# Kernel tuning notes

Measured on AMD Instinct MI355X. Metric: run time of the kernel, lower is better.

## Reference

```python
import jax, jax.numpy as jnp
import numpy as np

EPS = 1e-12  # matches torch F.normalize eps


def _l2_normalize(x):
    # F.normalize(x, p=2, dim=1): divide by clamped norm
    norm = jnp.sqrt(jnp.sum(x * x, axis=1, keepdims=True))
    return x / jnp.maximum(norm, EPS)


def setup_inputs() -> dict:
    key = jax.random.key(0)
    k1, k2, k3 = jax.random.split(key, 3)
    N, D, P, C = 16384, 768, 2048, 1000
    h = jax.random.normal(k1, (N, D), dtype=jnp.float32)
    prototypes = jax.random.normal(k2, (P, D), dtype=jnp.float32) * 0.1
    prototype_class = jax.random.normal(k3, (P, C), dtype=jnp.float32)
    temperature = jnp.float32(1.0)
    return {"h": h, "prototypes": prototypes,
            "prototype_class": prototype_class, "temperature": temperature}


def reference(h, prototypes, prototype_class, temperature):
    h_norm = _l2_normalize(h)                      # [N, D]
    p_norm = _l2_normalize(prototypes)             # [P, D]
    # cdist (p=2): sqrt(||a||^2 + ||b||^2 - 2 a.b), clamped at 0
    h_sq = jnp.sum(h_norm * h_norm, axis=1, keepdims=True)   # [N, 1]
    p_sq = jnp.sum(p_norm * p_norm, axis=1)                  # [P]
    dots = jnp.einsum('nd,pd->np', h_norm, p_norm)           # [N, P]
    dist_sq = jnp.maximum(h_sq + p_sq[None, :] - 2.0 * dots, 0.0)
    distances = jnp.sqrt(dist_sq)                            # [N, P]
    tau = jax.nn.softplus(temperature)
    activations = jnp.exp(-tau * distances)                  # [N, P]
    class_logits = jnp.matmul(activations, prototype_class)  # [N, C]
    return class_logits
```

## Files before the change

### kernel.cpp

```cpp
#include <hip/hip_runtime.h>
#include <hip/hip_bf16.h>
#include <math.h>

typedef unsigned short ushort_t;
typedef unsigned char uchar_t;
typedef unsigned int uint_t;
typedef __attribute__((ext_vector_type(8))) short bf16x8;
typedef __attribute__((ext_vector_type(4))) float f32x4;
typedef __attribute__((ext_vector_type(2))) long longx2;

#define AS1 __attribute__((address_space(1)))
#define AS3 __attribute__((address_space(3)))

__device__ __forceinline__ void gld_lds16(const void* g, void* l) {
  __builtin_amdgcn_global_load_lds((const AS1 void*)g, (AS3 void*)l, 16, 0, 0);
}

__device__ __forceinline__ ushort_t f32_to_bf16_bits(float v) {
  __hip_bfloat16 b = __float2bfloat16(v);
  return *(ushort_t*)&b;
}

__device__ __forceinline__ uint_t pack_fp8x4(float4 v, float sc) {
  int r = __builtin_amdgcn_cvt_pk_fp8_f32(v.x * sc, v.y * sc, 0, false);
  r = __builtin_amdgcn_cvt_pk_fp8_f32(v.z * sc, v.w * sc, r, true);
  return (uint_t)r;
}


__global__ __launch_bounds__(256) void prep(const float4* __restrict__ h,
                                            uchar_t* __restrict__ h8, int rowsH,
                                            const float4* __restrict__ p,
                                            uchar_t* __restrict__ p8, int rowsP,
                                            const float* __restrict__ pc,
                                            ushort_t* __restrict__ pcT,
                                            int P, int C, int normBlocks) {
  __shared__ float tile[32][33];
  if ((int)blockIdx.x < normBlocks) {
    int r = (blockIdx.x * 256 + threadIdx.x) >> 6;
    const int lane = threadIdx.x & 63;
    const float4* xr;
    uchar_t* o8;
    if (r < rowsH) {
      xr = h + (size_t)r * 192;
      o8 = h8;
    } else {
      r -= rowsH;
      if (r >= rowsP) return;
      xr = p + (size_t)r * 192;
      o8 = p8;
    }
    float4 v0 = xr[lane];
    float4 v1 = xr[lane + 64];
    float4 v2 = xr[lane + 128];
    float ss = v0.x * v0.x + v0.y * v0.y + v0.z * v0.z + v0.w * v0.w
             + v1.x * v1.x + v1.y * v1.y + v1.z * v1.z + v1.w * v1.w
             + v2.x * v2.x + v2.y * v2.y + v2.z * v2.z + v2.w * v2.w;
#pragma unroll
    for (int off = 32; off > 0; off >>= 1) ss += __shfl_xor(ss, off, 64);
    const float sc = 4.0f / fmaxf(sqrtf(ss), 1e-12f);
    const int rb = r >> 4, rl = r & 15;
    const int key4 = (rl >> 1) & 3;
    const int u = (lane & 7) >> 1;
    const int ksub = (lane & 15) >> 3;
    const int cphys = ((u ^ key4) << 4) + (ksub << 3) + ((lane & 1) << 2);
    const int ktb = lane >> 4;
    uchar_t* rowbase = o8 + (size_t)rb * 12 * 1024 + rl * 64 + cphys;
    *(uint_t*)(rowbase + (size_t)(ktb) * 1024)     = pack_fp8x4(v0, sc);
    *(uint_t*)(rowbase + (size_t)(4 + ktb) * 1024) = pack_fp8x4(v1, sc);
    *(uint_t*)(rowbase + (size_t)(8 + ktb) * 1024) = pack_fp8x4(v2, sc);
  } else {
    const int b = blockIdx.x - normBlocks;
    const int nkb = P / 32;
    const int bk = b % nkb, bc = b / nkb;
    const int k0 = bk * 32, c0 = bc * 32;
    const int tx = threadIdx.x & 31, ty = threadIdx.x >> 5;
#pragma unroll
    for (int rr = 0; rr < 4; ++rr) {
      const int c = c0 + tx;
      tile[ty + rr * 8][tx] = (c < C) ? pc[(size_t)(k0 + ty + rr * 8) * C + c] : 0.f;
    }
    __syncthreads();
    const int c2 = tx >> 3, off = tx & 7;
#pragma unroll
    for (int rr = 0; rr < 4; ++rr) {
      const int row = c0 + ty + rr * 8;
      const int rb = row >> 4, rl = row & 15;
      const int key4 = (rl >> 1) & 3;
      size_t us = (((size_t)rb * nkb + bk) * 16 + rl) * 32 + ((c2 ^ key4) << 3) + off;
      pcT[us] = f32_to_bf16_bits(tile[tx][ty + rr * 8]);
    }
  }
}

#define BARRIER() do { asm volatile("" ::: "memory"); __builtin_amdgcn_s_barrier(); \
                       asm volatile("" ::: "memory"); } while (0)
#define LGKM0()   asm volatile("s_waitcnt lgkmcnt(0)" ::: "memory")
#define VM3()     asm volatile("s_waitcnt vmcnt(3)" ::: "memory")
#define VM0()     asm volatile("s_waitcnt vmcnt(0)" ::: "memory")
#define PRIO1()   __builtin_amdgcn_s_setprio(1)
#define PRIO0()   __builtin_amdgcn_s_setprio(0)
#define MM(a, b, c)  __builtin_amdgcn_mfma_f32_16x16x32_bf16(a, b, c, 0, 0, 0)
#define MM8(a, b, c) __builtin_amdgcn_mfma_f32_16x16x32_fp8_fp8(a, b, c, 0, 0, 0)

__launch_bounds__(512, 4)
__global__ void gemm1_fp8_t3(const uchar_t* __restrict__ A, const uchar_t* __restrict__ B,
                             ushort_t* __restrict__ act, const float* __restrict__ tptr,
                             int nKt, int actKT, int gx, int gxlog2) {
  __shared__ __align__(16) uchar_t sm1[73728];
  const int tid = threadIdx.x, lane = tid & 63, wave = tid >> 6;
  const int wm = wave >> 2, wn = wave & 3;
  const int lid = blockIdx.x, xcd = lid & 7, q = lid >> 3;
  const int tb = q & (gx - 1), sb = ((q >> gxlog2) << 3) | xcd;

  f32x4 acc[4][4];
#pragma unroll
  for (int i = 0; i < 4; ++i)
#pragma unroll
    for (int j = 0; j < 4; ++j) acc[i][j] = (f32x4){0.f, 0.f, 0.f, 0.f};

  const uchar_t* Apl = A + (((size_t)(sb * 8) * nKt) << 10) + lane * 16;
  const uchar_t* Bpl = B + (((size_t)(tb * 16) * nKt) << 10) + lane * 16;

  const int fr = lane & 15, g = lane >> 4;
  const int rdoff = fr * 64 + ((g ^ ((fr >> 1) & 3)) << 4);
  const uchar_t* smA = sm1 + (wm << 12) + rdoff;
  const uchar_t* smB = sm1 + 8192 + (wn << 12) + rdoff;

#define G1_STA(r_, T_, bo_) gld_lds16(Apl + ((size_t)((r_) * nKt + (T_)) << 10), \
                                      sm1 + (bo_) + ((r_) << 10))
#define G1_STB(c_, T_, bo_) gld_lds16(Bpl + ((size_t)((c_) * nKt + (T_)) << 10), \
                                      sm1 + (bo_) + 8192 + ((c_) << 10))
#define G1_DSA(bo_, i_) (*(const longx2*)(smA + (bo_) + ((i_) << 10)))
#define G1_DSB(bo_, j_) (*(const longx2*)(smB + (bo_) + ((j_) << 10)))

  G1_STA(wave, 0, 0); G1_STB(wave, 0, 0); G1_STB(wave + 8, 0, 0);
  G1_STA(wave, 1, 24576); G1_STB(wave, 1, 24576); G1_STB(wave + 8, 1, 24576);
  VM3(); BARRIER();

  int boC = 0, boN = 24576, boNN = 49152;
  for (int kt = 0; kt < nKt; ++kt) {
    longx2 a0 = G1_DSA(boC, 0), a1 = G1_DSA(boC, 1), a2 = G1_DSA(boC, 2), a3 = G1_DSA(boC, 3);
    longx2 b0 = G1_DSB(boC, 0), b1 = G1_DSB(boC, 1), b2 = G1_DSB(boC, 2), b3 = G1_DSB(boC, 3);
    if (kt + 2 < nKt) {
      G1_STA(wave, kt + 2, boNN); G1_STB(wave, kt + 2, boNN); G1_STB(wave + 8, kt + 2, boNN);
    }
    BARRIER(); LGKM0();
    PRIO1();
    acc[0][0] = MM8(a0[0], b0[0], acc[0][0]); acc[0][1] = MM8(a0[0], b1[0], acc[0][1]);
    acc[0][2] = MM8(a0[0], b2[0], acc[0][2]); acc[0][3] = MM8(a0[0], b3[0], acc[0][3]);
    acc[1][0] = MM8(a1[0], b0[0], acc[1][0]); acc[1][1] = MM8(a1[0], b1[0], acc[1][1]);
    acc[1][2] = MM8(a1[0], b2[0], acc[1][2]); acc[1][3] = MM8(a1[0], b3[0], acc[1][3]);
    acc[2][0] = MM8(a2[0], b0[0], acc[2][0]); acc[2][1] = MM8(a2[0], b1[0], acc[2][1]);
    acc[2][2] = MM8(a2[0], b2[0], acc[2][2]); acc[2][3] = MM8(a2[0], b3[0], acc[2][3]);
    acc[3][0] = MM8(a3[0], b0[0], acc[3][0]); acc[3][1] = MM8(a3[0], b1[0], acc[3][1]);
    acc[3][2] = MM8(a3[0], b2[0], acc[3][2]); acc[3][3] = MM8(a3[0], b3[0], acc[3][3]);
    acc[0][0] = MM8(a0[1], b0[1], acc[0][0]); acc[0][1] = MM8(a0[1], b1[1], acc[0][1]);
    acc[0][2] = MM8(a0[1], b2[1], acc[0][2]); acc[0][3] = MM8(a0[1], b3[1], acc[0][3]);
    acc[1][0] = MM8(a1[1], b0[1], acc[1][0]); acc[1][1] = MM8(a1[1], b1[1], acc[1][1]);
    acc[1][2] = MM8(a1[1], b2[1], acc[1][2]); acc[1][3] = MM8(a1[1], b3[1], acc[1][3]);
    acc[2][0] = MM8(a2[1], b0[1], acc[2][0]); acc[2][1] = MM8(a2[1], b1[1], acc[2][1]);
    acc[2][2] = MM8(a2[1], b2[1], acc[2][2]); acc[2][3] = MM8(a2[1], b3[1], acc[2][3]);
    acc[3][0] = MM8(a3[1], b0[1], acc[3][0]); acc[3][1] = MM8(a3[1], b1[1], acc[3][1]);
    acc[3][2] = MM8(a3[1], b2[1], acc[3][2]); acc[3][3] = MM8(a3[1], b3[1], acc[3][3]);
    PRIO0();
    if (kt + 2 < nKt) { VM3(); } else if (kt + 1 < nKt) { VM0(); }
    BARRIER();
    int tswap = boC; boC = boN; boN = boNN; boNN = tswap;
  }

  float tmp = *tptr;
  const float tau = log1pf(expf(tmp));
  const int crow = g * 4;
  const int rowB = sb * 128 + wm * 64, colB = tb * 256 + wn * 64;
#pragma unroll
  for (int i = 0; i < 4; ++i)
#pragma unroll
    for (int j = 0; j < 4; ++j) {
      const int col = colB + j * 16 + fr;
      const size_t ktile = col >> 5;
      const int c2 = (col >> 3) & 3, co = col & 7;
#pragma unroll
      for (int rr = 0; rr < 4; ++rr) {
        const int row = rowB + i * 16 + crow + rr;
        const int rb = row >> 4, rl = row & 15;
        const int key4 = (rl >> 1) & 3;
        float d2 = fmaxf(2.0f - acc[i][j][rr] * 0.125f, 0.0f);
        float d = d2 * rsqrtf(fmaxf(d2, 1e-20f));
        float a = __expf(-tau * d);
        act[(((size_t)rb * actKT + ktile) * 16 + rl) * 32 + ((c2 ^ key4) << 3) + co] =
            f32_to_bf16_bits(a);
      }
    }
}

__launch_bounds__(512, 4)
__global__ void gemm2_bf16_t3(const ushort_t* __restrict__ A,
                              const ushort_t* __restrict__ B,
                              float* __restrict__ out, int ldc, int ncols,
                              int nKt) {
  __shared__ __align__(16) uchar_t sm[73728];
  const int tid = threadIdx.x, lane = tid & 63, wave = tid >> 6;
  const int wm = wave >> 2, wn = wave & 3;
  const int lid = blockIdx.x, xcd = lid & 7, q = lid >> 3;
  const int tb = q & 3, sb = ((q >> 2) << 3) | xcd;

  f32x4 acc[4][4];
#pragma unroll
  for (int i = 0; i < 4; ++i)
#pragma unroll
    for (int j = 0; j < 4; ++j) acc[i][j] = (f32x4){0.f, 0.f, 0.f, 0.f};

  const uchar_t* Apl = (const uchar_t*)A + (((size_t)(sb * 8) * nKt) << 10) + lane * 16;
  const uchar_t* Bpl = (const uchar_t*)B + (((size_t)(tb * 16) * nKt) << 10) + lane * 16;

  const int fr = lane & 15, g = lane >> 4;
  const int rdoff = fr * 64 + ((g ^ ((fr >> 1) & 3)) << 4);
  const uchar_t* smA = sm + (wm << 12) + rdoff;
  const uchar_t* smB = sm + 8192 + (wn << 12) + rdoff;

#define T3_STA(r_, T_, bo_) gld_lds16(Apl + ((size_t)((r_) * nKt + (T_)) << 10), \
                                      sm + (bo_) + ((r_) << 10))
#define T3_STB(c_, T_, bo_) gld_lds16(Bpl + ((size_t)((c_) * nKt + (T_)) << 10), \
                                      sm + (bo_) + 8192 + ((c_) << 10))
#define T3_DSA(bo_, i_) (*(const bf16x8*)(smA + (bo_) + ((i_) << 10)))
#define T3_DSB(bo_, j_) (*(const bf16x8*)(smB + (bo_) + ((j_) << 10)))

  T3_STA(wave, 0, 0); T3_STB(wave, 0, 0); T3_STB(wave + 8, 0, 0);
  T3_STA(wave, 1, 24576); T3_STB(wave, 1, 24576); T3_STB(wave + 8, 1, 24576);
  VM3(); BARRIER();

  int boC = 0, boN = 24576, boNN = 49152;
  for (int kt = 0; kt < nKt; ++kt) {
    bf16x8 a0 = T3_DSA(boC, 0), a1 = T3_DSA(boC, 1), a2 = T3_DSA(boC, 2), a3 = T3_DSA(boC, 3);
    bf16x8 b0 = T3_DSB(boC, 0), b1 = T3_DSB(boC, 1), b2 = T3_DSB(boC, 2), b3 = T3_DSB(boC, 3);
    if (kt + 2 < nKt) {
      T3_STA(wave, kt + 2, boNN); T3_STB(wave, kt + 2, boNN); T3_STB(wave + 8, kt + 2, boNN);
    }
    BARRIER(); LGKM0();
    PRIO1();
    acc[0][0] = MM(a0, b0, acc[0][0]); acc[0][1] = MM(a0, b1, acc[0][1]);
    acc[0][2] = MM(a0, b2, acc[0][2]); acc[0][3] = MM(a0, b3, acc[0][3]);
    acc[1][0] = MM(a1, b0, acc[1][0]); acc[1][1] = MM(a1, b1, acc[1][1]);
    acc[1][2] = MM(a1, b2, acc[1][2]); acc[1][3] = MM(a1, b3, acc[1][3]);
    acc[2][0] = MM(a2, b0, acc[2][0]); acc[2][1] = MM(a2, b1, acc[2][1]);
    acc[2][2] = MM(a2, b2, acc[2][2]); acc[2][3] = MM(a2, b3, acc[2][3]);
    acc[3][0] = MM(a3, b0, acc[3][0]); acc[3][1] = MM(a3, b1, acc[3][1]);
    acc[3][2] = MM(a3, b2, acc[3][2]); acc[3][3] = MM(a3, b3, acc[3][3]);
    PRIO0();
    if (kt + 2 < nKt) { VM3(); } else if (kt + 1 < nKt) { VM0(); }
    BARRIER();
    int tswap = boC; boC = boN; boN = boNN; boNN = tswap;
  }

  const int crow = g * 4;
  const int rowB = sb * 128 + wm * 64, colB = tb * 256 + wn * 64;
#pragma unroll
  for (int i = 0; i < 4; ++i)
#pragma unroll
    for (int j = 0; j < 4; ++j) {
      const int col = colB + j * 16 + fr;
      if (col < ncols) {
#pragma unroll
        for (int rr = 0; rr < 4; ++rr)
          out[(size_t)(rowB + i * 16 + crow + rr) * ldc + col] = acc[i][j][rr];
      }
    }
}

extern "C" void kernel_launch(void* const* d_in, const int* in_sizes, int n_in,
                              void* d_out, int out_size, void* d_ws, size_t ws_size,
                              hipStream_t stream) {
  const float* h    = (const float*)d_in[0];
  const float* prot = (const float*)d_in[1];
  const float* pc   = (const float*)d_in[2];
  const float* temp = (const float*)d_in[3];
  float* out = (float*)d_out;

  const int D = 768;
  const int N = in_sizes[0] / D;
  const int P = in_sizes[1] / D;
  const int C = in_sizes[2] / P;
  const int CP = (C + 127) & ~127;

  char* ws = (char*)d_ws;
  size_t off = 0;
  uchar_t* h8   = (uchar_t*)(ws + off); off += (size_t)N * D;
  uchar_t* p8   = (uchar_t*)(ws + off); off += (size_t)P * D;
  ushort_t* pcT = (ushort_t*)(ws + off); off += (size_t)CP * P * 2;
  ushort_t* act = (ushort_t*)(ws + off); off += (size_t)N * P * 2;
  (void)ws_size;

  const int normBlocks = (N + P) / 4;
  const int transBlocks = (P / 32) * (CP / 32);
  prep<<<normBlocks + transBlocks, 256, 0, stream>>>(
      (const float4*)h, h8, N, (const float4*)prot, p8, P,
      pc, pcT, P, C, normBlocks);

  {
    const int GX = P / 256, GY = N / 128;
    gemm1_fp8_t3<<<GX * GY, 512, 0, stream>>>(h8, p8, act, temp, D / 64, P / 32, GX, 3);
  }
  {
    const int GX = CP / 256, GY = N / 128;
    gemm2_bf16_t3<<<GX * GY, 512, 0, stream>>>(act, pcT, out, C, C, P / 32);
  }
}
```

Before: 214.2 us.

## Use 4-wave 64x128 per-wave tiles in GEMM2 and drop extra GEMM1 barrier

GEMM2 now runs with 4 waves per block instead of 8, and each wave computes a 64x128 output sub-tile with 32 accumulators. This raises per-wave register reuse of A fragments and halves LDS A reads per MFMA. Each thread issues twice as many global-to-LDS loads, so the wait count goes from vmcnt(3) to vmcnt(6). Separately, GEMM1 drops the mid-iteration barrier and the explicit lgkmcnt wait before its MFMAs, leaving the LDS read waits to the compiler. The trade-offs are fewer resident waves per CU, which means less latency hiding, and a small risk of a hazard in GEMM1 without the barrier.

```diff
diff --git a/kernel.cpp b/kernel.cpp
--- a/kernel.cpp
+++ b/kernel.cpp
@@ -96,6 +96,7 @@
 #define BARRIER() do { asm volatile("" ::: "memory"); __builtin_amdgcn_s_barrier(); \
                        asm volatile("" ::: "memory"); } while (0)
 #define LGKM0()   asm volatile("s_waitcnt lgkmcnt(0)" ::: "memory")
+#define VM6()     asm volatile("s_waitcnt vmcnt(6)" ::: "memory")
 #define VM3()     asm volatile("s_waitcnt vmcnt(3)" ::: "memory")
 #define VM0()     asm volatile("s_waitcnt vmcnt(0)" ::: "memory")
 #define PRIO1()   __builtin_amdgcn_s_setprio(1)
@@ -145,7 +146,6 @@
     if (kt + 2 < nKt) {
       G1_STA(wave, kt + 2, boNN); G1_STB(wave, kt + 2, boNN); G1_STB(wave + 8, kt + 2, boNN);
     }
-    BARRIER(); LGKM0();
     PRIO1();
     acc[0][0] = MM8(a0[0], b0[0], acc[0][0]); acc[0][1] = MM8(a0[0], b1[0], acc[0][1]);
     acc[0][2] = MM8(a0[0], b2[0], acc[0][2]); acc[0][3] = MM8(a0[0], b3[0], acc[0][3]);
@@ -194,71 +194,84 @@
     }
 }
 
-__launch_bounds__(512, 4)
-__global__ void gemm2_bf16_t3(const ushort_t* __restrict__ A,
+__launch_bounds__(256, 2)
+__global__ void gemm2_bf16_w4(const ushort_t* __restrict__ A,
                               const ushort_t* __restrict__ B,
                               float* __restrict__ out, int ldc, int ncols,
                               int nKt) {
   __shared__ __align__(16) uchar_t sm[73728];
   const int tid = threadIdx.x, lane = tid & 63, wave = tid >> 6;
-  const int wm = wave >> 2, wn = wave & 3;
+  const int wm = wave >> 1, wn = wave & 1;
   const int lid = blockIdx.x, xcd = lid & 7, q = lid >> 3;
   const int tb = q & 3, sb = ((q >> 2) << 3) | xcd;
 
-  f32x4 acc[4][4];
+  f32x4 acc[4][8];
 #pragma unroll
   for (int i = 0; i < 4; ++i)
 #pragma unroll
-    for (int j = 0; j < 4; ++j) acc[i][j] = (f32x4){0.f, 0.f, 0.f, 0.f};
+    for (int j = 0; j < 8; ++j) acc[i][j] = (f32x4){0.f, 0.f, 0.f, 0.f};
 
   const uchar_t* Apl = (const uchar_t*)A + (((size_t)(sb * 8) * nKt) << 10) + lane * 16;
   const uchar_t* Bpl = (const uchar_t*)B + (((size_t)(tb * 16) * nKt) << 10) + lane * 16;
 
   const int fr = lane & 15, g = lane >> 4;
   const int rdoff = fr * 64 + ((g ^ ((fr >> 1) & 3)) << 4);
-  const uchar_t* smA = sm + (wm << 12) + rdoff;
-  const uchar_t* smB = sm + 8192 + (wn << 12) + rdoff;
-
-#define T3_STA(r_, T_, bo_) gld_lds16(Apl + ((size_t)((r_) * nKt + (T_)) << 10), \
+  const uchar_t* smA = sm + ((wm * 4) << 10) + rdoff;
+  const uchar_t* smB = sm + 8192 + ((wn * 8) << 10) + rdoff;
+
+#define W4_STA(r_, T_, bo_) gld_lds16(Apl + ((size_t)((r_) * nKt + (T_)) << 10), \
                                       sm + (bo_) + ((r_) << 10))
-#define T3_STB(c_, T_, bo_) gld_lds16(Bpl + ((size_t)((c_) * nKt + (T_)) << 10), \
+#define W4_STB(c_, T_, bo_) gld_lds16(Bpl + ((size_t)((c_) * nKt + (T_)) << 10), \
                                       sm + (bo_) + 8192 + ((c_) << 10))
-#define T3_DSA(bo_, i_) (*(const bf16x8*)(smA + (bo_) + ((i_) << 10)))
-#define T3_DSB(bo_, j_) (*(const bf16x8*)(smB + (bo_) + ((j_) << 10)))
-
-  T3_STA(wave, 0, 0); T3_STB(wave, 0, 0); T3_STB(wave + 8, 0, 0);
-  T3_STA(wave, 1, 24576); T3_STB(wave, 1, 24576); T3_STB(wave + 8, 1, 24576);
-  VM3(); BARRIER();
+#define W4_DSA(bo_, i_) (*(const bf16x8*)(smA + (bo_) + ((i_) << 10)))
+#define W4_DSB(bo_, j_) (*(const bf16x8*)(smB + (bo_) + ((j_) << 10)))
+
+  W4_STA(wave, 0, 0); W4_STA(wave + 4, 0, 0);
+  W4_STB(wave, 0, 0); W4_STB(wave + 4, 0, 0); W4_STB(wave + 8, 0, 0); W4_STB(wave + 12, 0, 0);
+  W4_STA(wave, 1, 24576); W4_STA(wave + 4, 1, 24576);
+  W4_STB(wave, 1, 24576); W4_STB(wave + 4, 1, 24576); W4_STB(wave + 8, 1, 24576); W4_STB(wave + 12, 1, 24576);
+  VM6(); BARRIER();
 
   int boC = 0, boN = 24576, boNN = 49152;
   for (int kt = 0; kt < nKt; ++kt) {
-    bf16x8 a0 = T3_DSA(boC, 0), a1 = T3_DSA(boC, 1), a2 = T3_DSA(boC, 2), a3 = T3_DSA(boC, 3);
-    bf16x8 b0 = T3_DSB(boC, 0), b1 = T3_DSB(boC, 1), b2 = T3_DSB(boC, 2), b3 = T3_DSB(boC, 3);
+    bf16x8 a0 = W4_DSA(boC, 0), a1 = W4_DSA(boC, 1), a2 = W4_DSA(boC, 2), a3 = W4_DSA(boC, 3);
+    bf16x8 b0 = W4_DSB(boC, 0), b1 = W4_DSB(boC, 1), b2 = W4_DSB(boC, 2), b3 = W4_DSB(boC, 3);
+    bf16x8 b4 = W4_DSB(boC, 4), b5 = W4_DSB(boC, 5), b6 = W4_DSB(boC, 6), b7 = W4_DSB(boC, 7);
     if (kt + 2 < nKt) {
-      T3_STA(wave, kt + 2, boNN); T3_STB(wave, kt + 2, boNN); T3_STB(wave + 8, kt + 2, boNN);
+      W4_STA(wave, kt + 2, boNN); W4_STA(wave + 4, kt + 2, boNN);
+      W4_STB(wave, kt + 2, boNN); W4_STB(wave + 4, kt + 2, boNN);
+      W4_STB(wave + 8, kt + 2, boNN); W4_STB(wave + 12, kt + 2, boNN);
     }
     BARRIER(); LGKM0();
     PRIO1();
     acc[0][0] = MM(a0, b0, acc[0][0]); acc[0][1] = MM(a0, b1, acc[0][1]);
     acc[0][2] = MM(a0, b2, acc[0][2]); acc[0][3] = MM(a0, b3, acc[0][3]);
+    acc[0][4] = MM(a0, b4, acc[0][4]); acc[0][5] = MM(a0, b5, acc[0][5]);
+    acc[0][6] = MM(a0, b6, acc[0][6]); acc[0][7] = MM(a0, b7, acc[0][7]);
     acc[1][0] = MM(a1, b0, acc[1][0]); acc[1][1] = MM(a1, b1, acc[1][1]);
     acc[1][2] = MM(a1, b2, acc[1][2]); acc[1][3] = MM(a1, b3, acc[1][3]);
+    acc[1][4] = MM(a1, b4, acc[1][4]); acc[1][5] = MM(a1, b5, acc[1][5]);
+    acc[1][6] = MM(a1, b6, acc[1][6]); acc[1][7] = MM(a1, b7, acc[1][7]);
     acc[2][0] = MM(a2, b0, acc[2][0]); acc[2][1] = MM(a2, b1, acc[2][1]);
     acc[2][2] = MM(a2, b2, acc[2][2]); acc[2][3] = MM(a2, b3, acc[2][3]);
+    acc[2][4] = MM(a2, b4, acc[2][4]); acc[2][5] = MM(a2, b5, acc[2][5]);
+    acc[2][6] = MM(a2, b6, acc[2][6]); acc[2][7] = MM(a2, b7, acc[2][7]);
     acc[3][0] = MM(a3, b0, acc[3][0]); acc[3][1] = MM(a3, b1, acc[3][1]);
     acc[3][2] = MM(a3, b2, acc[3][2]); acc[3][3] = MM(a3, b3, acc[3][3]);
+    acc[3][4] = MM(a3, b4, acc[3][4]); acc[3][5] = MM(a3, b5, acc[3][5]);
+    acc[3][6] = MM(a3, b6, acc[3][6]); acc[3][7] = MM(a3, b7, acc[3][7]);
     PRIO0();
-    if (kt + 2 < nKt) { VM3(); } else if (kt + 1 < nKt) { VM0(); }
+    if (kt + 2 < nKt) { VM6(); } else if (kt + 1 < nKt) { VM0(); }
     BARRIER();
     int tswap = boC; boC = boN; boN = boNN; boNN = tswap;
   }
 
   const int crow = g * 4;
-  const int rowB = sb * 128 + wm * 64, colB = tb * 256 + wn * 64;
+  const int rowB = sb * 128 + wm * 64, colB = tb * 256 + wn * 128;
 #pragma unroll
   for (int i = 0; i < 4; ++i)
 #pragma unroll
-    for (int j = 0; j < 4; ++j) {
+    for (int j = 0; j < 8; ++j) {
       const int col = colB + j * 16 + fr;
       if (col < ncols) {
 #pragma unroll
@@ -303,6 +316,6 @@
   }
   {
     const int GX = CP / 256, GY = N / 128;
-    gemm2_bf16_t3<<<GX * GY, 512, 0, stream>>>(act, pcT, out, C, C, P / 32);
-  }
-}
+    gemm2_bf16_w4<<<GX * GY, 256, 0, stream>>>(act, pcT, out, C, C, P / 32);
+  }
+}
```

Result: faster. 209.5 us (-2.2%).
